# Optimization experiments

Measured on AMD Instinct MI355X. Metric: run time of the kernel, lower is better.

The kernel has to match this reference:

```python
import jax, jax.numpy as jnp
import numpy as np

TOP_K = 2

def setup_inputs() -> dict:
    key = jax.random.key(0)
    ks = jax.random.split(key, 8)
    B, S, D = 2, 2048, 1024
    N_r, N_s = 16, 2
    u = jax.random.normal(ks[0], (B, S, D), dtype=jnp.float32)
    centroids = jax.random.normal(ks[1], (N_r, D), dtype=jnp.float32)
    expert_biases = jnp.zeros((N_r,), dtype=jnp.float32)
    # routed expert Linear params: y = u @ W.T + b, W stored [E, d_out, d_in]
    Wr = jax.random.normal(ks[2], (N_r, D, D), dtype=jnp.float32) * (1.0 / np.sqrt(D))
    br = jax.random.normal(ks[3], (N_r, D), dtype=jnp.float32) * 0.01
    Ws = jax.random.normal(ks[4], (N_s, D, D), dtype=jnp.float32) * (1.0 / np.sqrt(D))
    bs = jax.random.normal(ks[5], (N_s, D), dtype=jnp.float32) * 0.01
    return {"u": u, "centroids": centroids, "expert_biases": expert_biases,
            "Wr": Wr, "br": br, "Ws": Ws, "bs": bs}

def reference(u, centroids, expert_biases, Wr, br, Ws, bs):
    N_r = centroids.shape[0]
    N_s = Ws.shape[0]
    # routing scores over experts
    raw_scores = jnp.einsum('bsd,ed->bse', u, centroids)          # [B,S,E]
    s = jax.nn.softmax(raw_scores + expert_biases, axis=-1)
    # scatter top-k softmax values (un-renormalized, as in the source) into gates
    topk_vals, topk_idx = jax.lax.top_k(s, TOP_K)                  # [B,S,K]
    g_topk = jnp.sum(jax.nn.one_hot(topk_idx, N_r, dtype=s.dtype) * topk_vals[..., None], axis=-2)  # [B,S,E]
    # dense per-expert Linear for all tokens, then gated combine (faithful to source)
    xe = jnp.einsum('bsd,eod->bseo', u, Wr) + br                   # [B,S,E,D]
    routed = jnp.einsum('bse,bseo->bso', g_topk, xe)               # [B,S,D]
    # shared experts: mean of N_s dense Linears
    shared = (jnp.einsum('bsd,eod->bso', u, Ws) + jnp.sum(bs, axis=0)) / N_s
    return u + routed + shared
```

## Files before the change

### kernel.cpp

```cpp
#include <hip/hip_runtime.h>

typedef unsigned short u16x8 __attribute__((ext_vector_type(8)));
typedef short          s16x8 __attribute__((ext_vector_type(8)));
typedef float          f32x4 __attribute__((ext_vector_type(4)));

#define NTOK   4096
#define DMODEL 1024
#define NEXP   16
#define TOPK   2
#define BKG    64
#define NKT    (DMODEL / BKG)
#define MAXT2  64

__device__ inline unsigned short f2bf(float f) {
    unsigned int x = __float_as_uint(f);
    x += 0x7fffu + ((x >> 16) & 1u);
    return (unsigned short)(x >> 16);
}
__device__ inline float bf2f(unsigned short h) {
    unsigned int x = ((unsigned int)h) << 16;
    return __uint_as_float(x);
}

__device__ inline void gld16(const void* g, void* l) {
    __builtin_amdgcn_global_load_lds(
        (const __attribute__((address_space(1))) void*)g,
        (__attribute__((address_space(3))) void*)l, 16, 0, 0);
}

#define NWR8  (NEXP * DMODEL * DMODEL / 8)
#define NWS8  (DMODEL * DMODEL / 8)
#define NB8   ((NEXP + 1) * DMODEL / 8)
#define RBLK  (NTOK / 4)
#define CBLK  ((NWR8 + NWS8 + NB8 + 255) / 256)

__global__ void prep_kernel(const float* __restrict__ u,
                            const float* __restrict__ cent,
                            const float* __restrict__ ebias,
                            const float* __restrict__ Wr,
                            const float* __restrict__ br,
                            const float* __restrict__ Ws,
                            const float* __restrict__ bs,
                            unsigned short* __restrict__ ub,
                            unsigned short* __restrict__ w17,
                            float* __restrict__ b17,
                            float* __restrict__ topk_g,
                            int*   __restrict__ topk_i) {
    int bid = blockIdx.x;
    if (bid >= RBLK) {
        int id = (bid - RBLK) * 256 + threadIdx.x;
        if (id < NWR8) {
            size_t base = (size_t)id * 8;
            f32x4 a = *(const f32x4*)&Wr[base];
            f32x4 b = *(const f32x4*)&Wr[base + 4];
            u16x8 o;
#pragma unroll
            for (int i = 0; i < 4; i++) { o[i] = f2bf(a[i]); o[i + 4] = f2bf(b[i]); }
            *(u16x8*)&w17[base] = o;
        } else if (id < NWR8 + NWS8) {
            size_t base = (size_t)(id - NWR8) * 8;
            f32x4 a0 = *(const f32x4*)&Ws[base];
            f32x4 b0 = *(const f32x4*)&Ws[base + 4];
            f32x4 a1 = *(const f32x4*)&Ws[(size_t)DMODEL * DMODEL + base];
            f32x4 b1 = *(const f32x4*)&Ws[(size_t)DMODEL * DMODEL + base + 4];
            u16x8 o;
#pragma unroll
            for (int i = 0; i < 4; i++) {
                o[i]     = f2bf(a0[i] + a1[i]);
                o[i + 4] = f2bf(b0[i] + b1[i]);
            }
            *(u16x8*)&w17[(size_t)NEXP * DMODEL * DMODEL + base] = o;
        } else if (id < NWR8 + NWS8 + NB8) {
            int base = (id - NWR8 - NWS8) * 8;
#pragma unroll
            for (int i = 0; i < 8; i++) {
                int idx = base + i;
                b17[idx] = idx < NEXP * DMODEL
                    ? br[idx]
                    : bs[idx - NEXP * DMODEL] + bs[idx - NEXP * DMODEL + DMODEL];
            }
        }
        return;
    }
    int wid  = threadIdx.x >> 6;
    int lane = threadIdx.x & 63;
    int t = bid * 4 + wid;
    const float* urow = u + (size_t)t * DMODEL;

    double acc[NEXP];
#pragma unroll
    for (int e = 0; e < NEXP; e++) acc[e] = 0.0;

    for (int j = 0; j < DMODEL / 64; j++) {
        int d = j * 64 + lane;
        float uf = urow[d];
        ub[(size_t)t * DMODEL + d] = f2bf(uf);
        double uv = (double)uf;
#pragma unroll
        for (int e = 0; e < NEXP; e++)
            acc[e] += uv * (double)cent[e * DMODEL + d];
    }
#pragma unroll
    for (int e = 0; e < NEXP; e++) {
        for (int off = 32; off; off >>= 1)
            acc[e] += __shfl_xor(acc[e], off);
    }
    if (lane == 0) {
        double mx = -1e300;
#pragma unroll
        for (int e = 0; e < NEXP; e++) {
            acc[e] += (double)ebias[e];
            if (acc[e] > mx) mx = acc[e];
        }
        double ex[NEXP], den = 0.0;
#pragma unroll
        for (int e = 0; e < NEXP; e++) { ex[e] = exp(acc[e] - mx); den += ex[e]; }
        int i1 = -1, i2 = -1;
        double v1 = -1.0, v2 = -1.0;
        for (int e = 0; e < NEXP; e++) {
            double v = ex[e];
            if (v > v1)      { v2 = v1; i2 = i1; v1 = v; i1 = e; }
            else if (v > v2) { v2 = v;  i2 = e; }
        }
        topk_g[t * 2 + 0] = (float)(v1 / den);
        topk_g[t * 2 + 1] = (float)(v2 / den);
        topk_i[t * 2 + 0] = i1;
        topk_i[t * 2 + 1] = i2;
    }
}

__global__ void bucket16(const float* __restrict__ tg,
                         const int*   __restrict__ ti,
                         int* __restrict__ cnt,
                         int* __restrict__ tokL,
                         float* __restrict__ gateL,
                         int* __restrict__ idL) {
    int e = blockIdx.x;
    __shared__ int base;
    if (threadIdx.x == 0) base = 0;
    __syncthreads();
    int lane = threadIdx.x & 63;
    for (int c0 = 0; c0 < NTOK * TOPK; c0 += 256) {
        int id = c0 + threadIdx.x;
        bool m = (ti[id] == e);
        unsigned long long mask = __ballot(m);
        int wcnt = __popcll(mask);
        int wpos = 0;
        if (lane == 0) wpos = atomicAdd(&base, wcnt);
        wpos = __shfl(wpos, 0);
        if (m) {
            int pos = wpos + __popcll(mask & ((1ull << lane) - 1ull));
            tokL[e * NTOK + pos]  = id >> 1;
            gateL[e * NTOK + pos] = tg[id];
            idL[e * NTOK + pos]   = id;
        }
    }
    __syncthreads();
    if (threadIdx.x == 0) cnt[e] = base;
}

__global__ __launch_bounds__(512, 2)
void moe_gemm(const unsigned short* __restrict__ ub,
              const unsigned short* __restrict__ w17,
              const float* __restrict__ b17,
              const int*   __restrict__ cnt,
              const int*   __restrict__ tokL,
              const float* __restrict__ gateL,
              const int*   __restrict__ idL,
              const float* __restrict__ u,
              float* __restrict__ out,
              unsigned short* __restrict__ y) {
    int bid = blockIdx.x;
    int np   = bid & 3;
    int tile = bid >> 2;
    int e, row0;
    if (tile < NTOK / 256) {
        e = NEXP; row0 = tile << 8;
    } else {
        int rt = tile - NTOK / 256;
        int ee = 0;
        for (; ee < NEXP; ee++) {
            int nt = (cnt[ee] + 255) >> 8;
            if (rt < nt) break;
            rt -= nt;
        }
        if (ee >= NEXP) return;
        e = ee; row0 = rt << 8;
    }
    bool is_shared = (e == NEXP);
    int count = is_shared ? NTOK : cnt[e];
    int n0 = np * 256;

    __shared__ __align__(16) unsigned short As[2][256 * BKG];
    __shared__ __align__(16) unsigned short Bs[2][256 * BKG];

    int t = threadIdx.x;
    int lane = t & 63, wid = t >> 6;
    int wm = wid >> 2, wn = wid & 3;
    int lr = lane & 15, lk4 = lane >> 4;

    int srow8 = lane >> 3;
    int scs   = ((lane & 7) ^ srow8) * 8;

    const int* tl = tokL + e * NTOK;
    int tokA[4];
#pragma unroll
    for (int r = 0; r < 4; r++) {
        int gi = row0 + r * 64 + wid * 8 + srow8;
        tokA[r] = is_shared ? gi : tl[gi < count ? gi : count - 1];
    }
    const unsigned short* bb = w17 + (size_t)e * DMODEL * DMODEL + (size_t)n0 * DMODEL;

#define STAGE(buf, kt) do {                                                        \
    int _k0 = (kt) * BKG;                                                          \
    _Pragma("unroll")                                                              \
    for (int r = 0; r < 4; r++) {                                                  \
        gld16(&ub[(size_t)tokA[r] * DMODEL + _k0 + scs],                           \
              &As[buf][(r * 64 + wid * 8) * BKG]);                                 \
        gld16(&bb[(size_t)(r * 64 + wid * 8 + srow8) * DMODEL + _k0 + scs],        \
              &Bs[buf][(r * 64 + wid * 8) * BKG]);                                 \
    } } while (0)

    f32x4 acc[8][4];
#pragma unroll
    for (int i = 0; i < 8; i++)
#pragma unroll
        for (int j = 0; j < 4; j++)
#pragma unroll
            for (int v = 0; v < 4; v++) acc[i][j][v] = 0.0f;

    STAGE(0, 0);
    int cur = 0;
    for (int kt = 0; kt < NKT; kt++) {
        if (kt + 1 < NKT) {
            STAGE(cur ^ 1, kt + 1);
            asm volatile("s_waitcnt vmcnt(8)" ::: "memory");
        } else {
            asm volatile("s_waitcnt vmcnt(0)" ::: "memory");
        }
        __builtin_amdgcn_s_barrier();

        __builtin_amdgcn_s_setprio(1);
#pragma unroll
        for (int ks = 0; ks < 2; ks++) {
            s16x8 b[4];
#pragma unroll
            for (int j = 0; j < 4; j++)
                b[j] = *(const s16x8*)&Bs[cur][(wn * 64 + j * 16 + lr) * BKG
                                               + (((ks * 4 + lk4) ^ (lr & 7)) * 8)];
#pragma unroll
            for (int i = 0; i < 8; i++) {
                s16x8 a = *(const s16x8*)&As[cur][(wm * 128 + i * 16 + lr) * BKG
                                                  + (((ks * 4 + lk4) ^ (lr & 7)) * 8)];
#pragma unroll
                for (int j = 0; j < 4; j++)
                    acc[i][j] = __builtin_amdgcn_mfma_f32_16x16x32_bf16(a, b[j], acc[i][j], 0, 0, 0);
            }
        }
        __builtin_amdgcn_s_setprio(0);

        asm volatile("" ::: "memory");
        __builtin_amdgcn_s_barrier();
        cur ^= 1;
    }
#undef STAGE

    const float* be = b17 + e * DMODEL;
    if (is_shared) {
#pragma unroll
        for (int i = 0; i < 8; i++) {
#pragma unroll
            for (int v = 0; v < 4; v++) {
                int row = row0 + wm * 128 + i * 16 + lk4 * 4 + v;
#pragma unroll
                for (int j = 0; j < 4; j++) {
                    int col = n0 + wn * 64 + j * 16 + lr;
                    size_t idx = (size_t)row * DMODEL + col;
                    out[idx] = u[idx] + 0.5f * (acc[i][j][v] + be[col]);
                }
            }
        }
    } else {
#pragma unroll
        for (int i = 0; i < 8; i++) {
#pragma unroll
            for (int v = 0; v < 4; v++) {
                int gi = row0 + wm * 128 + i * 16 + lk4 * 4 + v;
                if (gi < count) {
                    int id = idL[e * NTOK + gi];
                    float g = gateL[e * NTOK + gi];
                    unsigned short* yr = y + (size_t)id * DMODEL;
#pragma unroll
                    for (int j = 0; j < 4; j++) {
                        int col = n0 + wn * 64 + j * 16 + lr;
                        yr[col] = f2bf(g * (acc[i][j][v] + be[col]));
                    }
                }
            }
        }
    }
}

__global__ void combine_kernel(const unsigned short* __restrict__ y,
                               float* __restrict__ out) {
    int idx = blockIdx.x * 256 + threadIdx.x;
    int tk = idx >> 7;
    int d8 = (idx & 127) * 8;
    size_t base = (size_t)tk * DMODEL + d8;
    u16x8 a = *(const u16x8*)&y[(size_t)(tk * 2) * DMODEL + d8];
    u16x8 b = *(const u16x8*)&y[(size_t)(tk * 2 + 1) * DMODEL + d8];
    f32x4 o0 = *(const f32x4*)&out[base];
    f32x4 o1 = *(const f32x4*)&out[base + 4];
#pragma unroll
    for (int v = 0; v < 4; v++) {
        o0[v] += bf2f(a[v]) + bf2f(b[v]);
        o1[v] += bf2f(a[v + 4]) + bf2f(b[v + 4]);
    }
    *(f32x4*)&out[base] = o0;
    *(f32x4*)&out[base + 4] = o1;
}

extern "C" void kernel_launch(void* const* d_in, const int* in_sizes, int n_in,
                              void* d_out, int out_size, void* d_ws, size_t ws_size,
                              hipStream_t stream) {
    const float* u    = (const float*)d_in[0];
    const float* cent = (const float*)d_in[1];
    const float* eb   = (const float*)d_in[2];
    const float* Wr   = (const float*)d_in[3];
    const float* br   = (const float*)d_in[4];
    const float* Ws   = (const float*)d_in[5];
    const float* bs   = (const float*)d_in[6];
    float* out = (float*)d_out;

    char* ws = (char*)d_ws;
    size_t off = 0;
    auto take = [&](size_t b) { size_t o = off; off += (b + 255) & ~(size_t)255; return o; };
    float* topk_g = (float*)(ws + take(NTOK * TOPK * 4));
    int*   topk_i = (int*)  (ws + take(NTOK * TOPK * 4));
    int*   cnt    = (int*)  (ws + take(64 * 4));
    int*   tokL   = (int*)  (ws + take((size_t)NEXP * NTOK * 4));
    float* gateL  = (float*)(ws + take((size_t)NEXP * NTOK * 4));
    int*   idL    = (int*)  (ws + take((size_t)NEXP * NTOK * 4));
    float* b17    = (float*)(ws + take((size_t)(NEXP + 1) * DMODEL * 4));
    unsigned short* ub  = (unsigned short*)(ws + take((size_t)NTOK * DMODEL * 2));
    unsigned short* w17 = (unsigned short*)(ws + take((size_t)(NEXP + 1) * DMODEL * DMODEL * 2));
    unsigned short* y   = (unsigned short*)(ws + take((size_t)NTOK * TOPK * DMODEL * 2));

    prep_kernel<<<RBLK + CBLK, 256, 0, stream>>>(
        u, cent, eb, Wr, br, Ws, bs, ub, w17, b17, topk_g, topk_i);
    bucket16<<<NEXP, 256, 0, stream>>>(topk_g, topk_i, cnt, tokL, gateL, idL);
    moe_gemm<<<4 * MAXT2, 512, 0, stream>>>(
        ub, w17, b17, cnt, tokL, gateL, idL, u, out, y);
    combine_kernel<<<(NTOK * DMODEL / 8) / 256, 256, 0, stream>>>(y, out);
}
```

Baseline: 101.1 us.

## Shrink MoE GEMM tiles to 128x128 with two-wave blocks and BK=32

Replaces the 256x256 output tile, 8-wave block and BK=64 pipeline with a 128x128 tile computed by 2 waves, each covering all rows and 64 columns, with BK=32. The LDS swizzle is redone for 32-wide K rows and the per-row global source pointers are precomputed. The aim is many more, smaller blocks, for better load balance across CUs and across experts with uneven token counts. The cost is lower per-block arithmetic intensity, twice as many K iterations each ending in a barrier, and fewer waves per block to hide latency.

```diff
diff --git a/kernel.cpp b/kernel.cpp
--- a/kernel.cpp
+++ b/kernel.cpp
@@ -8,9 +8,9 @@
 #define DMODEL 1024
 #define NEXP   16
 #define TOPK   2
-#define BKG    64
-#define NKT    (DMODEL / BKG)
-#define MAXT2  64
+#define BK     32
+#define NK     (DMODEL / BK)
+#define MAXT   128
 
 __device__ inline unsigned short f2bf(float f) {
     unsigned int x = __float_as_uint(f);
@@ -159,7 +159,7 @@
     if (threadIdx.x == 0) cnt[e] = base;
 }
 
-__global__ __launch_bounds__(512, 2)
+__global__ __launch_bounds__(128, 2)
 void moe_gemm(const unsigned short* __restrict__ ub,
               const unsigned short* __restrict__ w17,
               const float* __restrict__ b17,
@@ -171,54 +171,55 @@
               float* __restrict__ out,
               unsigned short* __restrict__ y) {
     int bid = blockIdx.x;
-    int np   = bid & 3;
-    int tile = bid >> 2;
+    int tile = bid >> 3;
+    int n0 = (bid & 7) * 128;
     int e, row0;
-    if (tile < NTOK / 256) {
-        e = NEXP; row0 = tile << 8;
+    if (tile < NTOK / 128) {
+        e = NEXP; row0 = tile << 7;
     } else {
-        int rt = tile - NTOK / 256;
+        int rt = tile - NTOK / 128;
         int ee = 0;
         for (; ee < NEXP; ee++) {
-            int nt = (cnt[ee] + 255) >> 8;
+            int nt = (cnt[ee] + 127) >> 7;
             if (rt < nt) break;
             rt -= nt;
         }
         if (ee >= NEXP) return;
-        e = ee; row0 = rt << 8;
+        e = ee; row0 = rt << 7;
     }
     bool is_shared = (e == NEXP);
     int count = is_shared ? NTOK : cnt[e];
-    int n0 = np * 256;
-
-    __shared__ __align__(16) unsigned short As[2][256 * BKG];
-    __shared__ __align__(16) unsigned short Bs[2][256 * BKG];
+
+    __shared__ __align__(16) unsigned short As[2][128 * BK];
+    __shared__ __align__(16) unsigned short Bs[2][128 * BK];
 
     int t = threadIdx.x;
     int lane = t & 63, wid = t >> 6;
-    int wm = wid >> 2, wn = wid & 3;
     int lr = lane & 15, lk4 = lane >> 4;
-
-    int srow8 = lane >> 3;
-    int scs   = ((lane & 7) ^ srow8) * 8;
+    int rchunk = (lk4 ^ ((lr >> 1) & 3)) * 8;
+
+    int srow = lane >> 2;
+    int scs  = ((lane & 3) ^ ((lane >> 3) & 3)) * 8;
 
     const int* tl = tokL + e * NTOK;
-    int tokA[4];
-#pragma unroll
-    for (int r = 0; r < 4; r++) {
-        int gi = row0 + r * 64 + wid * 8 + srow8;
-        tokA[r] = is_shared ? gi : tl[gi < count ? gi : count - 1];
-    }
+    const unsigned short* asrc[4];
+    const unsigned short* bsrc[4];
     const unsigned short* bb = w17 + (size_t)e * DMODEL * DMODEL + (size_t)n0 * DMODEL;
-
-#define STAGE(buf, kt) do {                                                        \
-    int _k0 = (kt) * BKG;                                                          \
-    _Pragma("unroll")                                                              \
-    for (int r = 0; r < 4; r++) {                                                  \
-        gld16(&ub[(size_t)tokA[r] * DMODEL + _k0 + scs],                           \
-              &As[buf][(r * 64 + wid * 8) * BKG]);                                 \
-        gld16(&bb[(size_t)(r * 64 + wid * 8 + srow8) * DMODEL + _k0 + scs],        \
-              &Bs[buf][(r * 64 + wid * 8) * BKG]);                                 \
+#pragma unroll
+    for (int p = 0; p < 4; p++) {
+        int gi = row0 + wid * 64 + p * 16 + srow;
+        int tok = is_shared ? gi : tl[gi < count ? gi : count - 1];
+        asrc[p] = ub + (size_t)tok * DMODEL + scs;
+        bsrc[p] = bb + (size_t)(wid * 64 + p * 16 + srow) * DMODEL + scs;
+    }
+
+#define STAGE(buf, kt) do {                                                     \
+    int _k0 = (kt) * BK;                                                        \
+    _Pragma("unroll")                                                           \
+    for (int p = 0; p < 4; p++) {                                               \
+        int r = wid * 64 + p * 16;                                              \
+        gld16(asrc[p] + _k0, &As[buf][r * BK]);                                 \
+        gld16(bsrc[p] + _k0, &Bs[buf][r * BK]);                                 \
     } } while (0)
 
     f32x4 acc[8][4];
@@ -231,8 +232,8 @@
 
     STAGE(0, 0);
     int cur = 0;
-    for (int kt = 0; kt < NKT; kt++) {
-        if (kt + 1 < NKT) {
+    for (int kt = 0; kt < NK; kt++) {
+        if (kt + 1 < NK) {
             STAGE(cur ^ 1, kt + 1);
             asm volatile("s_waitcnt vmcnt(8)" ::: "memory");
         } else {
@@ -241,21 +242,16 @@
         __builtin_amdgcn_s_barrier();
 
         __builtin_amdgcn_s_setprio(1);
-#pragma unroll
-        for (int ks = 0; ks < 2; ks++) {
-            s16x8 b[4];
+        s16x8 b[4];
+#pragma unroll
+        for (int j = 0; j < 4; j++)
+            b[j] = *(const s16x8*)&Bs[cur][(wid * 64 + j * 16 + lr) * BK + rchunk];
+#pragma unroll
+        for (int i = 0; i < 8; i++) {
+            s16x8 a = *(const s16x8*)&As[cur][(i * 16 + lr) * BK + rchunk];
 #pragma unroll
             for (int j = 0; j < 4; j++)
-                b[j] = *(const s16x8*)&Bs[cur][(wn * 64 + j * 16 + lr) * BKG
-                                               + (((ks * 4 + lk4) ^ (lr & 7)) * 8)];
-#pragma unroll
-            for (int i = 0; i < 8; i++) {
-                s16x8 a = *(const s16x8*)&As[cur][(wm * 128 + i * 16 + lr) * BKG
-                                                  + (((ks * 4 + lk4) ^ (lr & 7)) * 8)];
-#pragma unroll
-                for (int j = 0; j < 4; j++)
-                    acc[i][j] = __builtin_amdgcn_mfma_f32_16x16x32_bf16(a, b[j], acc[i][j], 0, 0, 0);
-            }
+                acc[i][j] = __builtin_amdgcn_mfma_f32_16x16x32_bf16(a, b[j], acc[i][j], 0, 0, 0);
         }
         __builtin_amdgcn_s_setprio(0);
 
@@ -271,10 +267,10 @@
         for (int i = 0; i < 8; i++) {
 #pragma unroll
             for (int v = 0; v < 4; v++) {
-                int row = row0 + wm * 128 + i * 16 + lk4 * 4 + v;
+                int row = row0 + i * 16 + lk4 * 4 + v;
 #pragma unroll
                 for (int j = 0; j < 4; j++) {
-                    int col = n0 + wn * 64 + j * 16 + lr;
+                    int col = n0 + wid * 64 + j * 16 + lr;
                     size_t idx = (size_t)row * DMODEL + col;
                     out[idx] = u[idx] + 0.5f * (acc[i][j][v] + be[col]);
                 }
@@ -285,14 +281,14 @@
         for (int i = 0; i < 8; i++) {
 #pragma unroll
             for (int v = 0; v < 4; v++) {
-                int gi = row0 + wm * 128 + i * 16 + lk4 * 4 + v;
+                int gi = row0 + i * 16 + lk4 * 4 + v;
                 if (gi < count) {
                     int id = idL[e * NTOK + gi];
                     float g = gateL[e * NTOK + gi];
                     unsigned short* yr = y + (size_t)id * DMODEL;
 #pragma unroll
                     for (int j = 0; j < 4; j++) {
-                        int col = n0 + wn * 64 + j * 16 + lr;
+                        int col = n0 + wid * 64 + j * 16 + lr;
                         yr[col] = f2bf(g * (acc[i][j][v] + be[col]));
                     }
                 }
@@ -349,7 +345,7 @@
     prep_kernel<<<RBLK + CBLK, 256, 0, stream>>>(
         u, cent, eb, Wr, br, Ws, bs, ub, w17, b17, topk_g, topk_i);
     bucket16<<<NEXP, 256, 0, stream>>>(topk_g, topk_i, cnt, tokL, gateL, idL);
-    moe_gemm<<<4 * MAXT2, 512, 0, stream>>>(
+    moe_gemm<<<8 * MAXT, 128, 0, stream>>>(
         ub, w17, b17, cnt, tokL, gateL, idL, u, out, y);
     combine_kernel<<<(NTOK * DMODEL / 8) / 256, 256, 0, stream>>>(y, out);
 }
```

Result: slower. 118.2 us (+16.9%).
